# Kernel tuning notes

Hardware: AMD Instinct MI355X
Metric: run time of the kernel (lower is better)

The kernel has to match this reference:

```python
import jax, jax.numpy as jnp
import numpy as np

EPS = 1e-5


def setup_inputs() -> dict:
    key = jax.random.key(0)
    k1, k2, k3, k4 = jax.random.split(key, 4)
    C, H, W = 64, 512, 512
    return {
        "cont_feat": jax.random.normal(k1, (C, H, W), dtype=jnp.float32),
        "styl_feat": jax.random.normal(k2, (C, H, W), dtype=jnp.float32),
        "cont_seg": jax.random.randint(k3, (H, W), 0, 8, dtype=jnp.int32),
        "styl_seg": jax.random.randint(k4, (H, W), 0, 8, dtype=jnp.int32),
        "n_labels": 8,
    }


def _inv_sqrt_spectrum(e):
    # torch: keep eigenvalues >= 1e-5, d = e^-0.5 on kept, drop rest.
    keep = e >= EPS
    e_safe = jnp.where(keep, e, 1.0)
    return jnp.where(keep, e_safe ** -0.5, 0.0)


def _sqrt_spectrum(e):
    keep = e >= EPS
    e_safe = jnp.where(keep, e, 1.0)
    return jnp.where(keep, jnp.sqrt(e_safe), 0.0)


def _feature_wct(cont_feat, styl_feat, cont_seg, styl_seg, n_labels):
    """Segmentation-driven whitening-coloring transform (PhotoWCT.__feature_wct).

    For each label l: select content/style pixels with seg==l, whiten the
    content sub-features with (cov_c + I)^-1/2 (via symmetric eigendecomp ==
    torch.svd of a PSD matrix), color with cov_s^1/2, re-add style mean, and
    scatter back into the output. Masked weighted sums reproduce the
    index_select/index_copy_ math without data-dependent shapes.
    """
    C, H, W = cont_feat.shape
    Xc = cont_feat.reshape(C, -1)   # [C, Nc]
    Xs = styl_feat.reshape(C, -1)   # [C, Ns]
    cs = cont_seg.reshape(-1)
    ss = styl_seg.reshape(-1)
    I = jnp.eye(C, dtype=Xc.dtype)
    out = Xc
    for l in range(n_labels):  # fixed small label set; not a data-dim loop
        mc = (cs == l).astype(Xc.dtype)   # [Nc] content mask
        ms = (ss == l).astype(Xs.dtype)   # [Ns] style mask
        nc = mc.sum()
        ns = ms.sum()
        # label_indicator validity: both regions >10 px, size ratio <100
        valid = (nc > 10.0) & (ns > 10.0) & (nc < 100.0 * ns) & (ns < 100.0 * nc)
        # content: mean / centered / covariance (+I regularizer as in torch)
        mu_c = (Xc * mc).sum(axis=1) / jnp.maximum(nc, 1.0)
        Xcm = (Xc - mu_c[:, None]) * mc                       # [C, Nc] masked-centered
        div_c = jnp.where(nc - 1.0 == 0.0, EPS, nc - 1.0)
        cov_c = (Xcm @ Xcm.T) / div_c + I                     # [C, C]
        ec, vc = jnp.linalg.eigh(cov_c)
        Wh = (vc * _inv_sqrt_spectrum(ec)[None, :]) @ vc.T    # whitening [C, C]
        # style: mean / centered / covariance
        mu_s = (Xs * ms).sum(axis=1) / jnp.maximum(ns, 1.0)
        Xsm = (Xs - mu_s[:, None]) * ms
        div_s = jnp.where(ns - 1.0 == 0.0, EPS, ns - 1.0)
        cov_s = (Xsm @ Xsm.T) / div_s
        es, vs = jnp.linalg.eigh(cov_s)
        Co = (vs * _sqrt_spectrum(es)[None, :]) @ vs.T        # coloring [C, C]
        # apply fused transform to masked-centered content, re-add style mean
        y = (Co @ Wh) @ Xcm + mu_s[:, None]                   # [C, Nc]
        take = (mc > 0.0) & valid
        out = jnp.where(take[None, :], y, out)
    return out.reshape(1, C, H, W)


def reference(cont_feat, styl_feat, cont_seg, styl_seg, n_labels):
    return _feature_wct(cont_feat, styl_feat, cont_seg, styl_seg, n_labels)
```

## Files before the change

### kernel.cpp

```cpp
#include <hip/hip_runtime.h>
#include <math.h>

constexpr int NPIX  = 262144;
constexpr int NLAB  = 8;
constexpr int NITER = 5;

__host__ __device__ inline size_t offMpart()         { return 0; }
__host__ __device__ inline size_t offSpart(int nblk) { return (size_t)2*nblk*8*4096; }
__host__ __device__ inline size_t offCnt(int nblk)   { return offSpart(nblk) + (size_t)2*nblk*8*64; }
__host__ __device__ inline size_t offMR(int nblk)    { return offCnt(nblk) + (size_t)2*nblk*8; }
__host__ __device__ inline size_t offSR(int nblk)    { return offMR(nblk) + 2*8*4096; }
__host__ __device__ inline size_t offCR(int nblk)    { return offSR(nblk) + 2*8*64; }
__host__ __device__ inline size_t offWH(int nblk)    { return offCR(nblk) + 16; }
__host__ __device__ inline size_t offCO(int nblk)    { return offWH(nblk) + 8*4096; }
__host__ __device__ inline size_t offT(int nblk)     { return offCO(nblk) + 8*4096; }
__host__ __device__ inline size_t offBIAS(int nblk)  { return offT(nblk) + 8*4096; }
__host__ __device__ inline size_t offMUC(int nblk)   { return offBIAS(nblk) + 8*64; }
__host__ __device__ inline size_t offMUS(int nblk)   { return offMUC(nblk) + 8*64; }
__host__ __device__ inline size_t offVALID(int nblk) { return offMUS(nblk) + 8*64; }

__global__ __launch_bounds__(512, 2) void k_moments(
    const float* __restrict__ cont, const float* __restrict__ styl,
    const int* __restrict__ cseg, const int* __restrict__ sseg,
    float* __restrict__ ws, int nblk)
{
  const int t = blockIdx.y, blk = blockIdx.x;
  const float* __restrict__ X  = t ? styl : cont;
  const int*  __restrict__ seg = t ? sseg : cseg;
  const int tid = threadIdx.x, lane = tid & 63, wv = tid >> 6;

  __shared__ float xs[256 * 64];

  const int r0 = (lane >> 3) << 3;
  const int c0 = (lane & 7) << 3;

  float acc[8][8];
  #pragma unroll
  for (int i = 0; i < 8; ++i)
    #pragma unroll
    for (int j = 0; j < 8; ++j) acc[i][j] = 0.f;
  float ssum = 0.f;
  int   cnt  = 0;

  const int chunk = NPIX / nblk;
  const int pbase = blk * chunk;
  const int nph   = chunk >> 8;
  const int ci  = tid >> 5;
  const int pxi = (tid & 31) << 2;
  const int swW = (tid & 7) << 2;

  for (int ph = 0; ph < nph; ++ph) {
    const int p0 = pbase + (ph << 8);
    float4 v[8];
    #pragma unroll
    for (int q = 0; q < 8; ++q) {
      const int c  = ci + ((q & 3) << 4);
      const int px = pxi + ((q >> 2) << 7);
      v[q] = *reinterpret_cast<const float4*>(&X[(size_t)c * NPIX + p0 + px]);
    }
    int lb[4];
    #pragma unroll
    for (int g = 0; g < 4; ++g) lb[g] = seg[p0 + (g << 6) + lane];

    __syncthreads();
    #pragma unroll
    for (int q = 0; q < 8; ++q) {
      const int c  = ci + ((q & 3) << 4);
      const int px = pxi + ((q >> 2) << 7);
      const int pc = c ^ swW;
      xs[(px + 0) * 64 + pc] = v[q].x;
      xs[(px + 1) * 64 + pc] = v[q].y;
      xs[(px + 2) * 64 + pc] = v[q].z;
      xs[(px + 3) * 64 + pc] = v[q].w;
    }
    __syncthreads();

    for (int g = 0; g < 4; ++g) {
      unsigned long long m = __ballot(lb[g] == wv);
      cnt += __popcll(m);
      while (m) {
        const int j = (g << 6) + __builtin_ctzll(m);
        m &= m - 1;
        const int sw = j & 28;
        const float4 a0 = *reinterpret_cast<const float4*>(&xs[j * 64 + (r0 ^ sw)]);
        const float4 a1 = *reinterpret_cast<const float4*>(&xs[j * 64 + ((r0 ^ sw) ^ 4)]);
        const float4 b0 = *reinterpret_cast<const float4*>(&xs[j * 64 + (c0 ^ sw)]);
        const float4 b1 = *reinterpret_cast<const float4*>(&xs[j * 64 + ((c0 ^ sw) ^ 4)]);
        ssum += xs[j * 64 + (lane ^ sw)];
        const float av[8] = {a0.x, a0.y, a0.z, a0.w, a1.x, a1.y, a1.z, a1.w};
        const float bv[8] = {b0.x, b0.y, b0.z, b0.w, b1.x, b1.y, b1.z, b1.w};
        #pragma unroll
        for (int i = 0; i < 8; ++i)
          #pragma unroll
          for (int jj = 0; jj < 8; ++jj) acc[i][jj] += av[i] * bv[jj];
      }
    }
  }

  float* Md = ws + offMpart() + (size_t)((t * nblk + blk) * 8 + wv) * 4096;
  #pragma unroll
  for (int i = 0; i < 8; ++i) {
    *reinterpret_cast<float4*>(&Md[(r0 + i) * 64 + c0]) =
        make_float4(acc[i][0], acc[i][1], acc[i][2], acc[i][3]);
    *reinterpret_cast<float4*>(&Md[(r0 + i) * 64 + c0 + 4]) =
        make_float4(acc[i][4], acc[i][5], acc[i][6], acc[i][7]);
  }
  ws[offSpart(nblk) + (size_t)((t * nblk + blk) * 8 + wv) * 64 + lane] = ssum;
  if (lane == 0) ws[offCnt(nblk) + (size_t)(t * nblk + blk) * 8 + wv] = (float)cnt;
}

__global__ __launch_bounds__(256) void k_reduce(float* __restrict__ ws, int nblk)
{
  const int b = blockIdx.x;
  const int sgm = b & 15, tl = b >> 4, l = tl & 7, t = tl >> 3;
  const int tid = threadIdx.x;
  const int clen = nblk >> 3;
  const int c0 = blockIdx.y * clen, c1 = c0 + clen;
  const size_t stride = (size_t)8 * 4096;
  const float* src = ws + offMpart() + (size_t)(t * nblk) * stride + (size_t)l * 4096 + sgm * 256 + tid;
  float s0 = 0.f, s1 = 0.f, s2 = 0.f, s3 = 0.f;
  int bb = c0;
  for (; bb + 3 < c1; bb += 4) {
    s0 += src[(size_t)(bb + 0) * stride];
    s1 += src[(size_t)(bb + 1) * stride];
    s2 += src[(size_t)(bb + 2) * stride];
    s3 += src[(size_t)(bb + 3) * stride];
  }
  for (; bb < c1; ++bb) s0 += src[(size_t)bb * stride];
  atomicAdd(&ws[offMR(nblk) + (size_t)tl * 4096 + sgm * 256 + tid], (s0 + s1) + (s2 + s3));
  if (sgm == 0) {
    if (tid < 64) {
      float q0 = 0.f, q1 = 0.f;
      int b2 = c0;
      for (; b2 + 1 < c1; b2 += 2) {
        q0 += ws[offSpart(nblk) + (size_t)((t * nblk + b2) * 8 + l) * 64 + tid];
        q1 += ws[offSpart(nblk) + (size_t)((t * nblk + b2 + 1) * 8 + l) * 64 + tid];
      }
      for (; b2 < c1; ++b2)
        q0 += ws[offSpart(nblk) + (size_t)((t * nblk + b2) * 8 + l) * 64 + tid];
      atomicAdd(&ws[offSR(nblk) + tl * 64 + tid], q0 + q1);
    } else if (tid == 64) {
      float q = 0.f;
      for (int b2 = c0; b2 < c1; ++b2)
        q += ws[offCnt(nblk) + (size_t)(t * nblk + b2) * 8 + l];
      atomicAdd(&ws[offCR(nblk) + tl], q);
    }
  }
}

__device__ __forceinline__ void mm64x8(float* __restrict__ dst,
    const float* __restrict__ A, const float* __restrict__ B,
    int tid, float p0, float p1)
{
  const int r0 = (tid >> 4) << 1;
  const int c0 = (tid & 15) << 2;
  float acc[2][4];
  #pragma unroll
  for (int i = 0; i < 2; ++i)
    #pragma unroll
    for (int j = 0; j < 4; ++j) acc[i][j] = 0.f;
  #pragma unroll 4
  for (int k = 0; k < 64; ++k) {
    const float2 a = *reinterpret_cast<const float2*>(&A[k * 64 + r0]);
    const float4 b = *reinterpret_cast<const float4*>(&B[k * 64 + c0]);
    acc[0][0] += a.x * b.x; acc[0][1] += a.x * b.y;
    acc[0][2] += a.x * b.z; acc[0][3] += a.x * b.w;
    acc[1][0] += a.y * b.x; acc[1][1] += a.y * b.y;
    acc[1][2] += a.y * b.z; acc[1][3] += a.y * b.w;
  }
  #pragma unroll
  for (int i = 0; i < 2; ++i) {
    float4 o;
    o.x = p1 * acc[i][0] + (((r0 + i) == (c0 + 0)) ? p0 : 0.f);
    o.y = p1 * acc[i][1] + (((r0 + i) == (c0 + 1)) ? p0 : 0.f);
    o.z = p1 * acc[i][2] + (((r0 + i) == (c0 + 2)) ? p0 : 0.f);
    o.w = p1 * acc[i][3] + (((r0 + i) == (c0 + 3)) ? p0 : 0.f);
    *reinterpret_cast<float4*>(&dst[(r0 + i) * 64 + c0]) = o;
  }
}

__global__ __launch_bounds__(512) void k_ns(float* __restrict__ ws, int nblk)
{
  const int l = blockIdx.x & 7, t = blockIdx.x >> 3;
  const int tid = threadIdx.x;
  __shared__ float bA[4096], bY[4096], bZ[4096], bT[4096];
  float* svec   = bT;
  float* scal   = bT + 128;

  const float n0 = ws[offCR(nblk) + l];
  const float n1 = ws[offCR(nblk) + 8 + l];
  const float n = t ? n1 : n0;
  const bool valid = (n0 > 10.f) && (n1 > 10.f) && (n0 < 100.f * n1) && (n1 < 100.f * n0);
  if (tid < 64) svec[tid] = ws[offSR(nblk) + (t * 8 + l) * 64 + tid];
  __syncthreads();

  const float invn = 1.f / fmaxf(n, 1.f);
  const float nm1  = n - 1.f;
  const float rdiv = 1.f / ((nm1 == 0.f) ? 1e-5f : nm1);
  const int i0 = tid >> 3, jb = (tid & 7) << 3;
  const float Si = svec[i0];
  const float* MRp = ws + offMR(nblk) + (size_t)(t * 8 + l) * 4096;
  #pragma unroll
  for (int q = 0; q < 2; ++q) {
    const int j = jb + (q << 2);
    const float4 m  = *reinterpret_cast<const float4*>(&MRp[i0 * 64 + j]);
    const float4 sj = *reinterpret_cast<const float4*>(&svec[j]);
    float4 a;
    a.x = (m.x - Si * sj.x * invn) * rdiv + ((t == 0 && i0 == j + 0) ? 1.f : 0.f);
    a.y = (m.y - Si * sj.y * invn) * rdiv + ((t == 0 && i0 == j + 1) ? 1.f : 0.f);
    a.z = (m.z - Si * sj.z * invn) * rdiv + ((t == 0 && i0 == j + 2) ? 1.f : 0.f);
    a.w = (m.w - Si * sj.w * invn) * rdiv + ((t == 0 && i0 == j + 3) ? 1.f : 0.f);
    *reinterpret_cast<float4*>(&bA[i0 * 64 + j]) = a;
  }
  if (tid < 64) ws[(t ? offMUS(nblk) : offMUC(nblk)) + l * 64 + tid] = svec[tid] * invn;
  if (t == 0 && tid == 0) ws[offVALID(nblk) + l] = valid ? 1.f : 0.f;
  __syncthreads();

  if (tid < 64) {
    float s = 0.f;
    for (int j = 0; j < 64; ++j) s += fabsf(bA[j * 64 + tid]);
    #pragma unroll
    for (int o = 32; o; o >>= 1) s = fmaxf(s, __shfl_xor(s, o));
    if (tid == 0) scal[0] = fmaxf(s, 1e-20f);
  }
  __syncthreads();
  const float cval = scal[0];
  const float rc = 1.f / cval;

  #pragma unroll
  for (int q = 0; q < 2; ++q) {
    const int j = jb + (q << 2);
    float4 a = *reinterpret_cast<const float4*>(&bA[i0 * 64 + j]);
    a.x *= rc; a.y *= rc; a.z *= rc; a.w *= rc;
    *reinterpret_cast<float4*>(&bY[i0 * 64 + j]) = a;
    float4 z;
    z.x = (i0 == j + 0) ? 1.f : 0.f; z.y = (i0 == j + 1) ? 1.f : 0.f;
    z.z = (i0 == j + 2) ? 1.f : 0.f; z.w = (i0 == j + 3) ? 1.f : 0.f;
    *reinterpret_cast<float4*>(&bZ[i0 * 64 + j]) = z;
  }
  __syncthreads();

  float *Y = bY, *Z = bZ, *T = bT, *Wb = bA;
  for (int it = 0; it < NITER; ++it) {
    mm64x8(T, Z, Y, tid, 1.5f, -0.5f); __syncthreads();
    mm64x8(Wb, Y, T, tid, 0.f, 1.f);   __syncthreads();
    mm64x8(Y, T, Z, tid, 0.f, 1.f);    __syncthreads();
    float* nz = Y; Y = Wb; Wb = Z; Z = nz;
  }

  const float osc = t ? sqrtf(cval) : (1.0f / sqrtf(cval));
  const float* src = t ? Y : Z;
  float* dst = ws + (t ? offCO(nblk) : offWH(nblk)) + (size_t)l * 4096;
  #pragma unroll
  for (int q = 0; q < 2; ++q) {
    const int j = jb + (q << 2);
    float4 v = *reinterpret_cast<const float4*>(&src[i0 * 64 + j]);
    v.x *= osc; v.y *= osc; v.z *= osc; v.w *= osc;
    *reinterpret_cast<float4*>(&dst[i0 * 64 + j]) = v;
  }
}

__global__ __launch_bounds__(256) void k_tmat(float* __restrict__ ws, int nblk)
{
  const int l = blockIdx.x;
  const int tid = threadIdx.x;
  __shared__ float Am[4096], Bm[4096];
  __shared__ float red[64];
  __shared__ float mucS[64], musS[64];
  const bool valid = ws[offVALID(nblk) + l] > 0.5f;
  if (tid < 64) {
    red[tid] = 0.f;
    mucS[tid] = ws[offMUC(nblk) + l * 64 + tid];
    musS[tid] = ws[offMUS(nblk) + l * 64 + tid];
  }
  #pragma unroll
  for (int q = 0; q < 4; ++q) {
    const int e = tid * 4 + q * 1024;
    *reinterpret_cast<float4*>(&Am[e]) =
        *reinterpret_cast<const float4*>(&ws[offCO(nblk) + (size_t)l * 4096 + e]);
    *reinterpret_cast<float4*>(&Bm[e]) =
        *reinterpret_cast<const float4*>(&ws[offWH(nblk) + (size_t)l * 4096 + e]);
  }
  __syncthreads();
  const int lane = tid & 63, wv = tid >> 6;
  const int r0 = (wv << 4) + ((lane >> 4) << 2);
  const int c0 = (lane & 15) << 2;
  float acc[4][4];
  #pragma unroll
  for (int i = 0; i < 4; ++i)
    #pragma unroll
    for (int j = 0; j < 4; ++j) acc[i][j] = 0.f;
  #pragma unroll 4
  for (int k = 0; k < 64; ++k) {
    const float4 a = *reinterpret_cast<const float4*>(&Am[k * 64 + r0]);
    const float4 b = *reinterpret_cast<const float4*>(&Bm[k * 64 + c0]);
    const float av[4] = {a.x, a.y, a.z, a.w};
    const float bv[4] = {b.x, b.y, b.z, b.w};
    #pragma unroll
    for (int i = 0; i < 4; ++i)
      #pragma unroll
      for (int j = 0; j < 4; ++j) acc[i][j] += av[i] * bv[j];
  }
  float* Td = ws + offT(nblk) + (size_t)l * 4096;
  #pragma unroll
  for (int i = 0; i < 4; ++i) {
    float4 o;
    o.x = valid ? acc[i][0] : (((r0 + i) == (c0 + 0)) ? 1.f : 0.f);
    o.y = valid ? acc[i][1] : (((r0 + i) == (c0 + 1)) ? 1.f : 0.f);
    o.z = valid ? acc[i][2] : (((r0 + i) == (c0 + 2)) ? 1.f : 0.f);
    o.w = valid ? acc[i][3] : (((r0 + i) == (c0 + 3)) ? 1.f : 0.f);
    *reinterpret_cast<float4*>(&Td[(r0 + i) * 64 + c0]) = o;
    const float bp = o.x * mucS[c0] + o.y * mucS[c0 + 1] + o.z * mucS[c0 + 2] + o.w * mucS[c0 + 3];
    atomicAdd(&red[r0 + i], bp);
  }
  __syncthreads();
  if (tid < 64) ws[offBIAS(nblk) + l * 64 + tid] = valid ? (musS[tid] - red[tid]) : 0.f;
}

__global__ __launch_bounds__(512, 2) void k_apply(
    const float* __restrict__ cont, const int* __restrict__ cseg,
    const float* __restrict__ ws, float* __restrict__ out, int nblk)
{
  const int tid = threadIdx.x;
  const int p   = blockIdx.x * 512 + tid;
  __shared__ float Tq[8 * 1028];
  __shared__ float biasS[8 * 66];

  biasS[(tid >> 6) * 66 + (tid & 63)] = ws[offBIAS(nblk) + tid];

  const int lab = cseg[p];

#define DECLX(i) float4 X##i = make_float4(                               \
      cont[(size_t)(4 * i + 0) * NPIX + p],                               \
      cont[(size_t)(4 * i + 1) * NPIX + p],                               \
      cont[(size_t)(4 * i + 2) * NPIX + p],                               \
      cont[(size_t)(4 * i + 3) * NPIX + p]);
  DECLX(0)  DECLX(1)  DECLX(2)  DECLX(3)
  DECLX(4)  DECLX(5)  DECLX(6)  DECLX(7)
  DECLX(8)  DECLX(9)  DECLX(10) DECLX(11)
  DECLX(12) DECLX(13) DECLX(14) DECLX(15)
#undef DECLX

#define ACCX(i) {                                                         \
    const float4 tv =                                                     \
        *reinterpret_cast<const float4*>(&Trow[oc16 * 64 + 4 * i]);       \
    sa += tv.x * X##i.x + tv.y * X##i.y;                                  \
    sb += tv.z * X##i.z + tv.w * X##i.w; }

  const float* Tsrc = ws + offT(nblk);
  for (int q = 0; q < 4; ++q) {
    __syncthreads();
    #pragma unroll
    for (int ii = 0; ii < 4; ++ii) {
      const int f = tid + 512 * ii;
      const int ll = f >> 8;
      const int e4 = (f & 255) * 4;
      *reinterpret_cast<float4*>(&Tq[ll * 1028 + e4]) =
          *reinterpret_cast<const float4*>(&Tsrc[(size_t)ll * 4096 + q * 1024 + e4]);
    }
    __syncthreads();
    const float* Trow = &Tq[lab * 1028];
    #pragma unroll 2
    for (int oc16 = 0; oc16 < 16; ++oc16) {
      float sa = 0.f, sb = 0.f;
      ACCX(0)  ACCX(1)  ACCX(2)  ACCX(3)
      ACCX(4)  ACCX(5)  ACCX(6)  ACCX(7)
      ACCX(8)  ACCX(9)  ACCX(10) ACCX(11)
      ACCX(12) ACCX(13) ACCX(14) ACCX(15)
      const int oc = q * 16 + oc16;
      out[(size_t)oc * NPIX + p] = sa + sb + biasS[lab * 66 + oc];
    }
  }
#undef ACCX
}

extern "C" void kernel_launch(void* const* d_in, const int* in_sizes, int n_in,
                              void* d_out, int out_size, void* d_ws, size_t ws_size,
                              hipStream_t stream)
{
  const float* cont = (const float*)d_in[0];
  const float* styl = (const float*)d_in[1];
  const int*   cseg = (const int*)d_in[2];
  const int*   sseg = (const int*)d_in[3];
  float*       ws   = (float*)d_ws;
  float*       out  = (float*)d_out;

  const size_t favail = ws_size / 4;
  int nblk = 256;
  while (nblk > 8 && offVALID(nblk) + 8 > favail) nblk >>= 1;

  k_moments<<<dim3(nblk, 2), 512, 0, stream>>>(cont, styl, cseg, sseg, ws, nblk);
  hipMemsetAsync(ws + offMR(nblk), 0,
                 (offWH(nblk) - offMR(nblk)) * sizeof(float), stream);
  k_reduce<<<dim3(256, 8), 256, 0, stream>>>(ws, nblk);
  k_ns<<<dim3(16), 512, 0, stream>>>(ws, nblk);
  k_tmat<<<dim3(8), 256, 0, stream>>>(ws, nblk);
  k_apply<<<dim3(NPIX / 512), 512, 0, stream>>>(cont, cseg, ws, out, nblk);
}
```

Before: 357.2 us.

## Bucket pixels by label in apply kernel, process two same-label pixels per thread

The apply kernel now sorts the block's 512 pixels by segmentation label in shared memory (count, prefix, scatter) and pairs same-label pixels so each active thread handles two pixels. Each T row element read from LDS is reused for two pixels, and lanes in a wave tend to share a label, which reduces bank conflicts and LDS traffic. The cost is extra sync/atomic setup, gathered (uncoalesced) global loads and stores for the feature data, doubled register pressure (128 floats of inputs), and only about half the threads active in the matmul phase.

```diff
diff --git a/kernel.cpp b/kernel.cpp
--- a/kernel.cpp
+++ b/kernel.cpp
@@ -322,30 +322,71 @@
     const float* __restrict__ ws, float* __restrict__ out, int nblk)
 {
   const int tid = threadIdx.x;
-  const int p   = blockIdx.x * 512 + tid;
+  const int base = blockIdx.x * 512;
   __shared__ float Tq[8 * 1028];
   __shared__ float biasS[8 * 66];
-
+  __shared__ int labw[512];
+  __shared__ unsigned short sidx[520];
+  __shared__ int cnt8[8], cur8[8], offs8[8], npS;
+
+  if (tid < 8) cnt8[tid] = 0;
   biasS[(tid >> 6) * 66 + (tid & 63)] = ws[offBIAS(nblk) + tid];
-
-  const int lab = cseg[p];
-
-#define DECLX(i) float4 X##i = make_float4(                               \
-      cont[(size_t)(4 * i + 0) * NPIX + p],                               \
-      cont[(size_t)(4 * i + 1) * NPIX + p],                               \
-      cont[(size_t)(4 * i + 2) * NPIX + p],                               \
-      cont[(size_t)(4 * i + 3) * NPIX + p]);
-  DECLX(0)  DECLX(1)  DECLX(2)  DECLX(3)
-  DECLX(4)  DECLX(5)  DECLX(6)  DECLX(7)
-  DECLX(8)  DECLX(9)  DECLX(10) DECLX(11)
-  DECLX(12) DECLX(13) DECLX(14) DECLX(15)
-#undef DECLX
-
-#define ACCX(i) {                                                         \
+  __syncthreads();
+  {
+    const int lb = cseg[base + tid];
+    labw[tid] = lb;
+    atomicAdd(&cnt8[lb], 1);
+  }
+  __syncthreads();
+  if (tid == 0) {
+    int off = 0;
+    for (int l2 = 0; l2 < 8; ++l2) {
+      offs8[l2] = off; cur8[l2] = off;
+      off += cnt8[l2] + (cnt8[l2] & 1);
+    }
+    npS = off >> 1;
+  }
+  __syncthreads();
+  {
+    const int pos = atomicAdd(&cur8[labw[tid]], 1);
+    sidx[pos] = (unsigned short)tid;
+  }
+  __syncthreads();
+  if (tid < 8 && (cnt8[tid] & 1))
+    sidx[offs8[tid] + cnt8[tid]] = sidx[offs8[tid]];
+  __syncthreads();
+
+  const int np = npS;
+  const bool act = tid < np;
+  int p0 = base, p1 = base, lab = 0;
+  if (act) {
+    const int i0 = sidx[2 * tid], i1 = sidx[2 * tid + 1];
+    lab = labw[i0];
+    p0 = base + i0; p1 = base + i1;
+  }
+
+#define DECLXY(i) \
+  float4 X##i = make_float4(cont[(size_t)(4 * i + 0) * NPIX + p0],        \
+                            cont[(size_t)(4 * i + 1) * NPIX + p0],        \
+                            cont[(size_t)(4 * i + 2) * NPIX + p0],        \
+                            cont[(size_t)(4 * i + 3) * NPIX + p0]);      \
+  float4 Y##i = make_float4(cont[(size_t)(4 * i + 0) * NPIX + p1],        \
+                            cont[(size_t)(4 * i + 1) * NPIX + p1],        \
+                            cont[(size_t)(4 * i + 2) * NPIX + p1],        \
+                            cont[(size_t)(4 * i + 3) * NPIX + p1]);
+  DECLXY(0)  DECLXY(1)  DECLXY(2)  DECLXY(3)
+  DECLXY(4)  DECLXY(5)  DECLXY(6)  DECLXY(7)
+  DECLXY(8)  DECLXY(9)  DECLXY(10) DECLXY(11)
+  DECLXY(12) DECLXY(13) DECLXY(14) DECLXY(15)
+#undef DECLXY
+
+#define ACC2(i) {                                                         \
     const float4 tv =                                                     \
         *reinterpret_cast<const float4*>(&Trow[oc16 * 64 + 4 * i]);       \
     sa += tv.x * X##i.x + tv.y * X##i.y;                                  \
-    sb += tv.z * X##i.z + tv.w * X##i.w; }
+    sb += tv.z * X##i.z + tv.w * X##i.w;                                  \
+    ta += tv.x * Y##i.x + tv.y * Y##i.y;                                  \
+    tb += tv.z * Y##i.z + tv.w * Y##i.w; }
 
   const float* Tsrc = ws + offT(nblk);
   for (int q = 0; q < 4; ++q) {
@@ -359,19 +400,23 @@
           *reinterpret_cast<const float4*>(&Tsrc[(size_t)ll * 4096 + q * 1024 + e4]);
     }
     __syncthreads();
-    const float* Trow = &Tq[lab * 1028];
-    #pragma unroll 2
-    for (int oc16 = 0; oc16 < 16; ++oc16) {
-      float sa = 0.f, sb = 0.f;
-      ACCX(0)  ACCX(1)  ACCX(2)  ACCX(3)
-      ACCX(4)  ACCX(5)  ACCX(6)  ACCX(7)
-      ACCX(8)  ACCX(9)  ACCX(10) ACCX(11)
-      ACCX(12) ACCX(13) ACCX(14) ACCX(15)
-      const int oc = q * 16 + oc16;
-      out[(size_t)oc * NPIX + p] = sa + sb + biasS[lab * 66 + oc];
-    }
-  }
-#undef ACCX
+    if (act) {
+      const float* Trow = &Tq[lab * 1028];
+      #pragma unroll 2
+      for (int oc16 = 0; oc16 < 16; ++oc16) {
+        float sa = 0.f, sb = 0.f, ta = 0.f, tb = 0.f;
+        ACC2(0)  ACC2(1)  ACC2(2)  ACC2(3)
+        ACC2(4)  ACC2(5)  ACC2(6)  ACC2(7)
+        ACC2(8)  ACC2(9)  ACC2(10) ACC2(11)
+        ACC2(12) ACC2(13) ACC2(14) ACC2(15)
+        const int oc = q * 16 + oc16;
+        const float bs = biasS[lab * 66 + oc];
+        out[(size_t)oc * NPIX + p0] = sa + sb + bs;
+        out[(size_t)oc * NPIX + p1] = ta + tb + bs;
+      }
+    }
+  }
+#undef ACC2
 }
 
 extern "C" void kernel_launch(void* const* d_in, const int* in_sizes, int n_in,
```

Measured after the change: 382.5 us. 1.07x slower.
